# Optimization experiments

Measured on AMD Instinct MI355X. Metric: run time of the kernel, lower is better.

## Reference

```python
import jax, jax.numpy as jnp
import numpy as np

B, F_DIM, P, C, H = 16, 256, 8192, 96, 256


def setup_inputs() -> dict:
    key = jax.random.key(0)
    ks = jax.random.split(key, 8)
    seg_feat = jax.random.normal(ks[0], (B, F_DIM, P), dtype=jnp.float32)
    seg_label = jax.random.randint(ks[1], (B, P), 0, C, dtype=jnp.int64 if jax.config.read('jax_enable_x64') else jnp.int32)
    s1 = 1.0 / np.sqrt(F_DIM)
    s2 = 1.0 / np.sqrt(H)
    w1 = jax.random.uniform(ks[2], (F_DIM, H), jnp.float32, -s1, s1)
    b1 = jax.random.uniform(ks[3], (H,), jnp.float32, -s1, s1)
    w2 = jax.random.uniform(ks[4], (H, H), jnp.float32, -s2, s2)
    b2 = jax.random.uniform(ks[5], (H,), jnp.float32, -s2, s2)
    w_logit = jax.random.uniform(ks[6], (H, C), jnp.float32, -s2, s2)
    b_logit = jax.random.uniform(ks[7], (C,), jnp.float32, -s2, s2)
    return dict(seg_feat=seg_feat, seg_label=seg_label, w1=w1, b1=b1,
                w2=w2, b2=b2, w_logit=w_logit, b_logit=b_logit)


def _pool_by_class(seg_feat, seg_label, num_classes):
    # seg_feat: [B, F, P], seg_label: [B, P] -> pooled [B*C, F]
    b, f, p = seg_feat.shape
    seg_ids = (jnp.arange(b, dtype=seg_label.dtype)[:, None] * num_classes
               + seg_label).reshape(-1)                       # [B*P]
    feat = seg_feat.transpose(0, 2, 1).reshape(b * p, f)      # [B*P, F]
    segmax = jax.ops.segment_max(feat, seg_ids, num_segments=b * num_classes)
    counts = jax.ops.segment_sum(jnp.ones((b * p,), feat.dtype), seg_ids,
                                 num_segments=b * num_classes)  # [B*C]
    counts = counts[:, None]
    # torch: max over points of feat * onehot -> zeros from other classes
    # participate in the max unless the class covers ALL points; empty
    # classes pool to 0 (max of all zeros).
    pooled = jnp.where(counts == 0, 0.0,
                       jnp.where(counts == p, segmax, jnp.maximum(segmax, 0.0)))
    return pooled


def reference(seg_feat, seg_label, w1, b1, w2, b2, w_logit, b_logit):
    num_classes = w_logit.shape[1]
    pooled = _pool_by_class(seg_feat, seg_label, num_classes)   # [B*C, F]
    # feat_mlp: Linear+ReLU x2 (dropout_prob=0), then part_logit
    h = jax.nn.relu(pooled @ w1 + b1)
    h = jax.nn.relu(h @ w2 + b2)
    part_pred = h @ w_logit + b_logit                           # [B*C, C]
    b = seg_feat.shape[0]
    part_batch = jnp.repeat(jnp.arange(b), num_classes)
    part_label = jnp.tile(jnp.arange(num_classes), b)
    return part_pred, part_label, part_batch
```

## Files before the change

kernel.cpp:

```cpp
#include <hip/hip_runtime.h>

#define B 16
#define F_DIM 256
#define P 8192
#define C 96
#define H 256
#define NSEG (B * C)
#define G 8
#define NFBLK (F_DIM / G)

__device__ __forceinline__ unsigned f2key(float x) {
    unsigned u = __float_as_uint(x);
    return (u & 0x80000000u) ? ~u : (u | 0x80000000u);
}
__device__ __forceinline__ float key2f(unsigned k) {
    unsigned u = (k & 0x80000000u) ? (k & 0x7FFFFFFFu) : ~k;
    return __uint_as_float(u);
}

__global__ __launch_bounds__(256) void pool_kernel(const float* __restrict__ feat,
                                                   const int* __restrict__ label,
                                                   float* __restrict__ pooled) {
    __shared__ unsigned smax[G][C];
    __shared__ int hist[C];
    const int blk = blockIdx.x;
    const int b = blk >> 5;
    const int f0 = (blk & 31) << 3;
    const int t = threadIdx.x;

    for (int i = t; i < G * C; i += 256) ((unsigned*)smax)[i] = 0u;
    if (t < C) hist[t] = 0;
    __syncthreads();

    const int4* lrow4 = (const int4*)(label + (size_t)b * P);
    int4 lab[8];
    #pragma unroll
    for (int j = 0; j < 8; ++j) lab[j] = lrow4[t + j * 256];

    #pragma unroll
    for (int j = 0; j < 8; ++j) {
        atomicAdd(&hist[lab[j].x], 1);
        atomicAdd(&hist[lab[j].y], 1);
        atomicAdd(&hist[lab[j].z], 1);
        atomicAdd(&hist[lab[j].w], 1);
    }

    const float4* fbase4 = (const float4*)(feat + ((size_t)b * F_DIM + f0) * P);

    float4 cur[8], nxt[8];
    #pragma unroll
    for (int j = 0; j < 8; ++j) cur[j] = fbase4[t + j * 256];

    #pragma unroll 1
    for (int f = 0; f < G; ++f) {
        if (f + 1 < G) {
            #pragma unroll
            for (int j = 0; j < 8; ++j)
                nxt[j] = fbase4[(size_t)(f + 1) * (P / 4) + t + j * 256];
        }
        #pragma unroll
        for (int j = 0; j < 8; ++j) {
            atomicMax(&smax[f][lab[j].x], f2key(cur[j].x));
            atomicMax(&smax[f][lab[j].y], f2key(cur[j].y));
            atomicMax(&smax[f][lab[j].z], f2key(cur[j].z));
            atomicMax(&smax[f][lab[j].w], f2key(cur[j].w));
        }
        #pragma unroll
        for (int j = 0; j < 8; ++j) cur[j] = nxt[j];
    }
    __syncthreads();

    if (t < C) {
        const int cnt = hist[t];
        float4 lo, hi;
        float* lv = (float*)&lo;
        float* hv = (float*)&hi;
        #pragma unroll
        for (int f = 0; f < 4; ++f) {
            const float v = key2f(smax[f][t]);
            lv[f] = (cnt == 0) ? 0.0f : ((cnt == P) ? v : fmaxf(v, 0.0f));
        }
        #pragma unroll
        for (int f = 4; f < 8; ++f) {
            const float v = key2f(smax[f][t]);
            hv[f - 4] = (cnt == 0) ? 0.0f : ((cnt == P) ? v : fmaxf(v, 0.0f));
        }
        float* dst = &pooled[(size_t)(b * C + t) * F_DIM + f0];
        *(float4*)dst = lo;
        *(float4*)(dst + 4) = hi;
    }
}

template <int COLS, int RELU, int OUTW>
__global__ __launch_bounds__(256, 3) void dense_kernel(const float* __restrict__ x,
                                                       const float* __restrict__ w,
                                                       const float* __restrict__ bias,
                                                       float* __restrict__ y,
                                                       float* __restrict__ tails) {
    constexpr int NQ = COLS / 4;
    __shared__ float xs[8][H];
    __shared__ float ps[8][COLS][17];
    const int t = threadIdx.x;
    const int row0 = blockIdx.x * 8;
    const int bj0 = blockIdx.y * COLS;

    {
        int i0 = t, i1 = t + 256;
        ((float4*)xs)[i0] = ((const float4*)(x + (size_t)row0 * H))[i0];
        ((float4*)xs)[i1] = ((const float4*)(x + (size_t)row0 * H))[i1];
    }
    __syncthreads();

    const int s = t >> 4;
    const int jq = t & 15;

    if (jq < NQ) {
        const float4* w4 = (const float4*)w;
        constexpr int WS4 = OUTW / 4;
        const int wq = (bj0 >> 2) + jq;
        const int kbase = s * 16;
        float4 acc[8];
        #pragma unroll
        for (int r = 0; r < 8; ++r) acc[r] = (float4){0.f, 0.f, 0.f, 0.f};

        #pragma unroll
        for (int i = 0; i < 16; ++i) {
            const int k = kbase + i;
            const float4 wv = w4[k * WS4 + wq];
            #pragma unroll
            for (int r = 0; r < 8; ++r) {
                const float xv = xs[r][k];
                acc[r].x = fmaf(xv, wv.x, acc[r].x);
                acc[r].y = fmaf(xv, wv.y, acc[r].y);
                acc[r].z = fmaf(xv, wv.z, acc[r].z);
                acc[r].w = fmaf(xv, wv.w, acc[r].w);
            }
        }
        #pragma unroll
        for (int r = 0; r < 8; ++r) {
            ps[r][jq * 4 + 0][s] = acc[r].x;
            ps[r][jq * 4 + 1][s] = acc[r].y;
            ps[r][jq * 4 + 2][s] = acc[r].z;
            ps[r][jq * 4 + 3][s] = acc[r].w;
        }
    }
    __syncthreads();

    for (int e = t; e < 8 * COLS; e += 256) {
        const int r = e / COLS, j = e % COLS;
        float v = bias[bj0 + j];
        #pragma unroll
        for (int q = 0; q < 16; ++q) v += ps[r][j][q];
        if (RELU) v = fmaxf(v, 0.0f);
        y[(size_t)(row0 + r) * OUTW + bj0 + j] = v;
    }

    if (tails != nullptr && t < 8) {
        const int row = row0 + t;
        tails[row] = (float)(row % C);
        tails[NSEG + row] = (float)(row / C);
    }
}

extern "C" void kernel_launch(void* const* d_in, const int* in_sizes, int n_in,
                              void* d_out, int out_size, void* d_ws, size_t ws_size,
                              hipStream_t stream) {
    const float* feat  = (const float*)d_in[0];
    const int*   label = (const int*)d_in[1];
    const float* w1    = (const float*)d_in[2];
    const float* b1    = (const float*)d_in[3];
    const float* w2    = (const float*)d_in[4];
    const float* b2    = (const float*)d_in[5];
    const float* wl    = (const float*)d_in[6];
    const float* bl    = (const float*)d_in[7];
    float* out = (float*)d_out;

    char* ws = (char*)d_ws;
    float* pooled = (float*)ws;
    float* h1     = (float*)(ws + NSEG * H * 4);
    float* h2     = (float*)(ws + 2 * NSEG * H * 4);

    pool_kernel<<<B * NFBLK, 256, 0, stream>>>(feat, label, pooled);
    dense_kernel<64, 1, H><<<dim3(NSEG / 8, 4), 256, 0, stream>>>(pooled, w1, b1, h1, nullptr);
    dense_kernel<64, 1, H><<<dim3(NSEG / 8, 4), 256, 0, stream>>>(h1, w2, b2, h2, nullptr);
    dense_kernel<48, 0, C><<<dim3(NSEG / 8, 2), 256, 0, stream>>>(h2, wl, bl, out, out + (size_t)NSEG * C);
}
```

Before: 44.32 us.

## Split pooling over point quarters and merge partial maxima in first dense layer

The pool kernel now splits each (batch, feature-group) block into four point ranges, launching four times more blocks, each handling a quarter of the points. Each block writes raw ordered-key partial maxima and per-quarter class counts to workspace. The first dense layer reduces the four partials, sums the counts and applies the empty/full-class masking while loading its input tile. This is meant to raise occupancy and memory-level parallelism in the bandwidth-bound pooling pass, at the cost of extra workspace traffic and a heavier load phase in the first dense kernel.

Measured after the change: 44.42 us. About the same (+0.2%).

```diff
diff --git a/kernel.cpp b/kernel.cpp
--- a/kernel.cpp
+++ b/kernel.cpp
@@ -8,6 +8,8 @@
 #define NSEG (B * C)
 #define G 8
 #define NFBLK (F_DIM / G)
+#define SPLIT 4
+#define PQ (P / SPLIT)
 
 __device__ __forceinline__ unsigned f2key(float x) {
     unsigned u = __float_as_uint(x);
@@ -20,79 +22,76 @@
 
 __global__ __launch_bounds__(256) void pool_kernel(const float* __restrict__ feat,
                                                    const int* __restrict__ label,
-                                                   float* __restrict__ pooled) {
+                                                   unsigned* __restrict__ kbuf,
+                                                   int* __restrict__ cnts) {
     __shared__ unsigned smax[G][C];
     __shared__ int hist[C];
     const int blk = blockIdx.x;
-    const int b = blk >> 5;
-    const int f0 = (blk & 31) << 3;
+    const int q  = blk & 3;
+    const int fg = (blk >> 2) & 31;
+    const int b  = blk >> 7;
+    const int f0 = fg << 3;
     const int t = threadIdx.x;
 
     for (int i = t; i < G * C; i += 256) ((unsigned*)smax)[i] = 0u;
     if (t < C) hist[t] = 0;
     __syncthreads();
 
-    const int4* lrow4 = (const int4*)(label + (size_t)b * P);
-    int4 lab[8];
-    #pragma unroll
-    for (int j = 0; j < 8; ++j) lab[j] = lrow4[t + j * 256];
-
-    #pragma unroll
-    for (int j = 0; j < 8; ++j) {
-        atomicAdd(&hist[lab[j].x], 1);
-        atomicAdd(&hist[lab[j].y], 1);
-        atomicAdd(&hist[lab[j].z], 1);
-        atomicAdd(&hist[lab[j].w], 1);
-    }
-
-    const float4* fbase4 = (const float4*)(feat + ((size_t)b * F_DIM + f0) * P);
-
-    float4 cur[8], nxt[8];
-    #pragma unroll
-    for (int j = 0; j < 8; ++j) cur[j] = fbase4[t + j * 256];
+    const int4* lrow4 = (const int4*)(label + (size_t)b * P + (size_t)q * PQ);
+    int4 lab[2];
+    lab[0] = lrow4[t];
+    lab[1] = lrow4[t + 256];
+
+    if (fg == 0) {
+        #pragma unroll
+        for (int j = 0; j < 2; ++j) {
+            atomicAdd(&hist[lab[j].x], 1);
+            atomicAdd(&hist[lab[j].y], 1);
+            atomicAdd(&hist[lab[j].z], 1);
+            atomicAdd(&hist[lab[j].w], 1);
+        }
+    }
+
+    const float4* fbase4 = (const float4*)(feat + ((size_t)b * F_DIM + f0) * P + (size_t)q * PQ);
+
+    float4 cur[2], nxt[2];
+    cur[0] = fbase4[t];
+    cur[1] = fbase4[t + 256];
 
     #pragma unroll 1
     for (int f = 0; f < G; ++f) {
         if (f + 1 < G) {
-            #pragma unroll
-            for (int j = 0; j < 8; ++j)
-                nxt[j] = fbase4[(size_t)(f + 1) * (P / 4) + t + j * 256];
-        }
-        #pragma unroll
-        for (int j = 0; j < 8; ++j) {
+            nxt[0] = fbase4[(size_t)(f + 1) * (P / 4) + t];
+            nxt[1] = fbase4[(size_t)(f + 1) * (P / 4) + t + 256];
+        }
+        #pragma unroll
+        for (int j = 0; j < 2; ++j) {
             atomicMax(&smax[f][lab[j].x], f2key(cur[j].x));
             atomicMax(&smax[f][lab[j].y], f2key(cur[j].y));
             atomicMax(&smax[f][lab[j].z], f2key(cur[j].z));
             atomicMax(&smax[f][lab[j].w], f2key(cur[j].w));
         }
-        #pragma unroll
-        for (int j = 0; j < 8; ++j) cur[j] = nxt[j];
-    }
-    __syncthreads();
+        cur[0] = nxt[0];
+        cur[1] = nxt[1];
+    }
+    __syncthreads();
+
+    if (fg == 0 && t < C) cnts[q * NSEG + b * C + t] = hist[t];
 
     if (t < C) {
-        const int cnt = hist[t];
-        float4 lo, hi;
-        float* lv = (float*)&lo;
-        float* hv = (float*)&hi;
-        #pragma unroll
-        for (int f = 0; f < 4; ++f) {
-            const float v = key2f(smax[f][t]);
-            lv[f] = (cnt == 0) ? 0.0f : ((cnt == P) ? v : fmaxf(v, 0.0f));
-        }
-        #pragma unroll
-        for (int f = 4; f < 8; ++f) {
-            const float v = key2f(smax[f][t]);
-            hv[f - 4] = (cnt == 0) ? 0.0f : ((cnt == P) ? v : fmaxf(v, 0.0f));
-        }
-        float* dst = &pooled[(size_t)(b * C + t) * F_DIM + f0];
-        *(float4*)dst = lo;
-        *(float4*)(dst + 4) = hi;
-    }
-}
-
-template <int COLS, int RELU, int OUTW>
+        uint4 lo, hi;
+        lo.x = smax[0][t]; lo.y = smax[1][t]; lo.z = smax[2][t]; lo.w = smax[3][t];
+        hi.x = smax[4][t]; hi.y = smax[5][t]; hi.z = smax[6][t]; hi.w = smax[7][t];
+        unsigned* dst = kbuf + (size_t)q * NSEG * F_DIM + (size_t)(b * C + t) * F_DIM + f0;
+        *(uint4*)dst = lo;
+        *(uint4*)(dst + 4) = hi;
+    }
+}
+
+template <int COLS, int RELU, int OUTW, int POOLIN>
 __global__ __launch_bounds__(256, 3) void dense_kernel(const float* __restrict__ x,
+                                                       const unsigned* __restrict__ kx,
+                                                       const int* __restrict__ cnts,
                                                        const float* __restrict__ w,
                                                        const float* __restrict__ bias,
                                                        float* __restrict__ y,
@@ -104,7 +103,35 @@
     const int row0 = blockIdx.x * 8;
     const int bj0 = blockIdx.y * COLS;
 
-    {
+    if (POOLIN) {
+        const uint4* k4 = (const uint4*)kx;
+        const size_t base = (size_t)row0 * (H / 4);
+        #pragma unroll
+        for (int jj = 0; jj < 2; ++jj) {
+            const int i = t + jj * 256;
+            uint4 km = k4[base + i];
+            #pragma unroll
+            for (int h = 1; h < SPLIT; ++h) {
+                const uint4 kh = k4[(size_t)h * NSEG * (H / 4) + base + i];
+                km.x = km.x > kh.x ? km.x : kh.x;
+                km.y = km.y > kh.y ? km.y : kh.y;
+                km.z = km.z > kh.z ? km.z : kh.z;
+                km.w = km.w > kh.w ? km.w : kh.w;
+            }
+            const int row = row0 + (i >> 6);
+            const int cnt = cnts[row] + cnts[NSEG + row] +
+                            cnts[2 * NSEG + row] + cnts[3 * NSEG + row];
+            float4 v;
+            v.x = key2f(km.x); v.y = key2f(km.y); v.z = key2f(km.z); v.w = key2f(km.w);
+            if (cnt == 0) {
+                v.x = v.y = v.z = v.w = 0.0f;
+            } else if (cnt != P) {
+                v.x = fmaxf(v.x, 0.0f); v.y = fmaxf(v.y, 0.0f);
+                v.z = fmaxf(v.z, 0.0f); v.w = fmaxf(v.w, 0.0f);
+            }
+            ((float4*)xs)[i] = v;
+        }
+    } else {
         int i0 = t, i1 = t + 256;
         ((float4*)xs)[i0] = ((const float4*)(x + (size_t)row0 * H))[i0];
         ((float4*)xs)[i1] = ((const float4*)(x + (size_t)row0 * H))[i1];
@@ -176,12 +203,14 @@
     float* out = (float*)d_out;
 
     char* ws = (char*)d_ws;
-    float* pooled = (float*)ws;
-    float* h1     = (float*)(ws + NSEG * H * 4);
-    float* h2     = (float*)(ws + 2 * NSEG * H * 4);
-
-    pool_kernel<<<B * NFBLK, 256, 0, stream>>>(feat, label, pooled);
-    dense_kernel<64, 1, H><<<dim3(NSEG / 8, 4), 256, 0, stream>>>(pooled, w1, b1, h1, nullptr);
-    dense_kernel<64, 1, H><<<dim3(NSEG / 8, 4), 256, 0, stream>>>(h1, w2, b2, h2, nullptr);
-    dense_kernel<48, 0, C><<<dim3(NSEG / 8, 2), 256, 0, stream>>>(h2, wl, bl, out, out + (size_t)NSEG * C);
-}
+    const size_t KBYTES = (size_t)SPLIT * NSEG * H * 4;
+    unsigned* kbuf = (unsigned*)ws;
+    int*      cnts = (int*)(ws + KBYTES);
+    float*    h1   = (float*)(ws + KBYTES + 32768);
+    float*    h2   = (float*)(ws + KBYTES + 32768 + (size_t)NSEG * H * 4);
+
+    pool_kernel<<<B * NFBLK * SPLIT, 256, 0, stream>>>(feat, label, kbuf, cnts);
+    dense_kernel<64, 1, H, 1><<<dim3(NSEG / 8, 4), 256, 0, stream>>>(nullptr, kbuf, cnts, w1, b1, h1, nullptr);
+    dense_kernel<64, 1, H, 0><<<dim3(NSEG / 8, 4), 256, 0, stream>>>(h1, nullptr, nullptr, w2, b2, h2, nullptr);
+    dense_kernel<48, 0, C, 0><<<dim3(NSEG / 8, 2), 256, 0, stream>>>(h2, nullptr, nullptr, wl, bl, out, out + (size_t)NSEG * C);
+}
```
